# Kernel optimization log

Hardware: AMD Instinct MI355X
Metric: run time of the kernel (lower is better)

Reference implementation:

```python
import jax, jax.numpy as jnp
import numpy as np

N_NODES = 50000
N_EDGES = 600000
D_IN = 128
H = D_IN // 2  # 64
N_GRAPHS = 500
DIM_TARGET = 1


def setup_inputs() -> dict:
    key = jax.random.key(0)
    ks = jax.random.split(key, 16)
    x = jax.random.normal(ks[0], (N_NODES, D_IN), dtype=jnp.float32)
    edge_index = jax.random.randint(ks[1], (2, N_EDGES), 0, N_NODES, dtype=jnp.int64)
    batch = jnp.sort(jax.random.randint(ks[2], (N_NODES,), 0, N_GRAPHS, dtype=jnp.int64))
    # SAGEConv params: lin_l (neighbor aggregate, with bias), lin_r (root, no bias)
    s = 1.0 / np.sqrt(D_IN)
    Wl = jax.random.uniform(ks[3], (D_IN, H), jnp.float32, -s, s)
    bl = jnp.zeros((H,), jnp.float32)
    Wr = jax.random.uniform(ks[4], (D_IN, H), jnp.float32, -s, s)
    # MLP: 64->32->16->8->1
    dims = [H, H // 2, H // 4, H // 8, DIM_TARGET]
    params = {}
    for i in range(4):
        si = 1.0 / np.sqrt(dims[i])
        params[f"W{i}"] = jax.random.uniform(ks[5 + 2 * i], (dims[i], dims[i + 1]), jnp.float32, -si, si)
        params[f"b{i}"] = jax.random.uniform(ks[6 + 2 * i], (dims[i + 1],), jnp.float32, -si, si)
    return dict(x=x, edge_index=edge_index, batch=batch, Wl=Wl, bl=bl, Wr=Wr, **params)


def reference(x, edge_index, batch, Wl, bl, Wr, W0, b0, W1, b1, W2, b2, W3, b3):
    n_nodes = x.shape[0]
    src, dst = edge_index[0], edge_index[1]
    # SAGEConv mean aggregation: mean of source-node features at each target node
    agg = jax.ops.segment_sum(x[src], dst, num_segments=n_nodes)          # [N, D]
    cnt = jax.ops.segment_sum(jnp.ones((src.shape[0],), x.dtype), dst, num_segments=n_nodes)
    mean_nbr = agg / jnp.maximum(cnt, 1.0)[:, None]
    x1 = mean_nbr @ Wl + bl + x @ Wr                                      # [N, H]
    # global_mean_pool by graph id
    gsum = jax.ops.segment_sum(x1, batch, num_segments=N_GRAPHS)          # [G, H]
    gcnt = jax.ops.segment_sum(jnp.ones((n_nodes,), x.dtype), batch, num_segments=N_GRAPHS)
    h = gsum / jnp.maximum(gcnt, 1.0)[:, None]
    # MLP (dropout is identity in eval mode)
    h = jax.nn.relu(h @ W0 + b0)
    h = jax.nn.relu(h @ W1 + b1)
    h = jax.nn.relu(h @ W2 + b2)
    return h @ W3 + b3
```

## Files before the change

### kernel.cpp

```cpp
#include <hip/hip_runtime.h>
#include <hip/hip_bf16.h>

#define N_NODES  50000
#define N_EDGES  600000
#define D_IN     128
#define H        64
#define N_GRAPHS 500
#define MAXDEG   48

#define CONV_BLOCKS 6250
#define SCAT_CHUNKS 512
#define SCAT_BLOCKS (SCAT_CHUNKS * 8)
#define EPC         1172
#define NPS         (N_NODES / 8)
#define GST_BLOCKS  2
#define SPLIT       8

__device__ __forceinline__ float bflo(unsigned int u) { return __uint_as_float(u << 16); }
__device__ __forceinline__ float bfhi(unsigned int u) { return __uint_as_float(u & 0xffff0000u); }

__global__ __launch_bounds__(256) void prep_kernel(
        const float* __restrict__ x, unsigned short* __restrict__ xb,
        const int* __restrict__ src, const int* __restrict__ dst,
        int* __restrict__ deg, unsigned short* __restrict__ col,
        const int* __restrict__ batch, int* __restrict__ gstart) {
    int bid = blockIdx.x, t = threadIdx.x;
    if (bid < CONV_BLOCKS) {
        int i = bid * 256 + t;
        float4 f = ((const float4*)x)[i];
        ushort4 u;
        u.x = __bfloat16_as_ushort(__float2bfloat16(f.x));
        u.y = __bfloat16_as_ushort(__float2bfloat16(f.y));
        u.z = __bfloat16_as_ushort(__float2bfloat16(f.z));
        u.w = __bfloat16_as_ushort(__float2bfloat16(f.w));
        ((ushort4*)xb)[i] = u;
    } else if (bid < CONV_BLOCKS + SCAT_BLOCKS) {
        int rel   = bid - CONV_BLOCKS;
        int shard = bid & 7;
        int chunk = rel >> 3;
        int lo = shard * NPS, hi = lo + NPS;
        int e0 = chunk * EPC;
        int e1 = e0 + EPC; if (e1 > N_EDGES) e1 = N_EDGES;
        for (int e = e0 + t; e < e1; e += 256) {
            int d = dst[e];
            if (d >= lo && d < hi) {
                int pos = atomicAdd(&deg[d], 1);
                if (pos < MAXDEG)
                    col[(size_t)d * MAXDEG + pos] = (unsigned short)src[e];
            }
        }
    } else {
        int g = (bid - CONV_BLOCKS - SCAT_BLOCKS) * 256 + t;
        if (g <= N_GRAPHS) {
            int lo = 0, hi = N_NODES;
            while (lo < hi) {
                int m = (lo + hi) >> 1;
                if (batch[m] < g) lo = m + 1; else hi = m;
            }
            gstart[g] = lo;
        }
    }
}

__global__ __launch_bounds__(256) void gather_kernel(
        const unsigned short* __restrict__ xb, const unsigned short* __restrict__ col,
        const int* __restrict__ deg, const int* __restrict__ gstart,
        float* __restrict__ Pn, float* __restrict__ Px, int* __restrict__ gcnt) {
    __shared__ float red[4 * D_IN];
    int bid  = blockIdx.x;
    int wave = threadIdx.x >> 6;
    int lane = threadIdx.x & 63;

    if (bid < N_GRAPHS * SPLIT) {
        int g = bid >> 3;
        int s = bid & 7;
        int n0 = gstart[g], n1 = gstart[g + 1];
        const unsigned short* xl = xb + 2 * lane;

        float2 pn = make_float2(0.f, 0.f);
        for (int n = n0 + s * 4 + wave; n < n1; n += 4 * SPLIT) {
            int d = deg[n];
            int dl = (d < MAXDEG) ? d : MAXDEG;
            const unsigned short* cl = col + (size_t)n * MAXDEG;
            int cidx = (lane < dl) ? (int)cl[lane] : 0;

            float2 t = make_float2(0.f, 0.f);
            int j = 0;
            for (; j + 8 <= dl; j += 8) {
                int s0 = __shfl(cidx, j),     s1 = __shfl(cidx, j + 1);
                int s2 = __shfl(cidx, j + 2), s3 = __shfl(cidx, j + 3);
                int s4 = __shfl(cidx, j + 4), s5 = __shfl(cidx, j + 5);
                int s6 = __shfl(cidx, j + 6), s7 = __shfl(cidx, j + 7);
                unsigned int u0 = *(const unsigned int*)(xl + (size_t)s0 * D_IN);
                unsigned int u1 = *(const unsigned int*)(xl + (size_t)s1 * D_IN);
                unsigned int u2 = *(const unsigned int*)(xl + (size_t)s2 * D_IN);
                unsigned int u3 = *(const unsigned int*)(xl + (size_t)s3 * D_IN);
                unsigned int u4 = *(const unsigned int*)(xl + (size_t)s4 * D_IN);
                unsigned int u5 = *(const unsigned int*)(xl + (size_t)s5 * D_IN);
                unsigned int u6 = *(const unsigned int*)(xl + (size_t)s6 * D_IN);
                unsigned int u7 = *(const unsigned int*)(xl + (size_t)s7 * D_IN);
                t.x += bflo(u0) + bflo(u1) + bflo(u2) + bflo(u3)
                     + bflo(u4) + bflo(u5) + bflo(u6) + bflo(u7);
                t.y += bfhi(u0) + bfhi(u1) + bfhi(u2) + bfhi(u3)
                     + bfhi(u4) + bfhi(u5) + bfhi(u6) + bfhi(u7);
            }
            for (; j + 4 <= dl; j += 4) {
                int s0 = __shfl(cidx, j),     s1 = __shfl(cidx, j + 1);
                int s2 = __shfl(cidx, j + 2), s3 = __shfl(cidx, j + 3);
                unsigned int u0 = *(const unsigned int*)(xl + (size_t)s0 * D_IN);
                unsigned int u1 = *(const unsigned int*)(xl + (size_t)s1 * D_IN);
                unsigned int u2 = *(const unsigned int*)(xl + (size_t)s2 * D_IN);
                unsigned int u3 = *(const unsigned int*)(xl + (size_t)s3 * D_IN);
                t.x += bflo(u0) + bflo(u1) + bflo(u2) + bflo(u3);
                t.y += bfhi(u0) + bfhi(u1) + bfhi(u2) + bfhi(u3);
            }
            for (; j < dl; ++j) {
                int sn = __shfl(cidx, j);
                unsigned int u = *(const unsigned int*)(xl + (size_t)sn * D_IN);
                t.x += bflo(u); t.y += bfhi(u);
            }
            if (d > 0) {
                float w = __builtin_amdgcn_rcpf((float)d);
                pn.x = fmaf(t.x, w, pn.x);
                pn.y = fmaf(t.y, w, pn.y);
            }
        }
        red[wave * D_IN + 2 * lane]     = pn.x;
        red[wave * D_IN + 2 * lane + 1] = pn.y;
        __syncthreads();
        if (threadIdx.x < D_IN) {
            float v = red[threadIdx.x] + red[D_IN + threadIdx.x]
                    + red[2 * D_IN + threadIdx.x] + red[3 * D_IN + threadIdx.x];
            atomicAdd(&Pn[g * D_IN + threadIdx.x], v);
        }
    } else {
        int p  = bid - N_GRAPHS * SPLIT;
        int n0 = gstart[p], n1 = gstart[p + 1];
        float fx = 0.f, fy = 0.f;
        for (int n = n0 + wave; n < n1; n += 4) {
            unsigned int u = *(const unsigned int*)(xb + (size_t)n * D_IN + 2 * lane);
            fx += bflo(u); fy += bfhi(u);
        }
        red[wave * D_IN + 2 * lane]     = fx;
        red[wave * D_IN + 2 * lane + 1] = fy;
        __syncthreads();
        if (threadIdx.x < D_IN) {
            float v = red[threadIdx.x] + red[D_IN + threadIdx.x]
                    + red[2 * D_IN + threadIdx.x] + red[3 * D_IN + threadIdx.x];
            Px[p * D_IN + threadIdx.x] = v;
        }
        if (threadIdx.x == 0) gcnt[p] = n1 - n0;
    }
}

__global__ void final_kernel(
        const float* __restrict__ Pn, const float* __restrict__ Px,
        const int* __restrict__ gcnt,
        const float* __restrict__ Wl, const float* __restrict__ bl,
        const float* __restrict__ Wr,
        const float* __restrict__ W0, const float* __restrict__ b0,
        const float* __restrict__ W1, const float* __restrict__ b1,
        const float* __restrict__ W2, const float* __restrict__ b2,
        const float* __restrict__ W3, const float* __restrict__ b3,
        float* __restrict__ out) {
    int g = blockIdx.x;
    int t = threadIdx.x;
    __shared__ float sp[D_IN], sx[D_IN], h[H], a0[32], a1[16], a2[8];
    sp[t]      = Pn[g * D_IN + t];
    sp[t + 64] = Pn[g * D_IN + 64 + t];
    sx[t]      = Px[g * D_IN + t];
    sx[t + 64] = Px[g * D_IN + 64 + t];
    __syncthreads();

    int ng = gcnt[g];
    float acc = 0.f;
    #pragma unroll 8
    for (int d = 0; d < D_IN; ++d)
        acc += sp[d] * Wl[d * H + t] + sx[d] * Wr[d * H + t];
    h[t] = (ng > 0) ? (acc / (float)ng + bl[t]) : 0.f;
    __syncthreads();

    if (t < 32) { float a = b0[t]; for (int d = 0; d < H;  ++d) a += h[d]  * W0[d * 32 + t]; a0[t] = fmaxf(a, 0.f); }
    __syncthreads();
    if (t < 16) { float a = b1[t]; for (int d = 0; d < 32; ++d) a += a0[d] * W1[d * 16 + t]; a1[t] = fmaxf(a, 0.f); }
    __syncthreads();
    if (t < 8)  { float a = b2[t]; for (int d = 0; d < 16; ++d) a += a1[d] * W2[d * 8 + t];  a2[t] = fmaxf(a, 0.f); }
    __syncthreads();
    if (t == 0) { float a = b3[0]; for (int d = 0; d < 8;  ++d) a += a2[d] * W3[d]; out[g] = a; }
}

extern "C" void kernel_launch(void* const* d_in, const int* in_sizes, int n_in,
                              void* d_out, int out_size, void* d_ws, size_t ws_size,
                              hipStream_t stream) {
    const float* x     = (const float*)d_in[0];
    const int*   ei    = (const int*)  d_in[1];
    const int*   batch = (const int*)  d_in[2];
    const float* Wl    = (const float*)d_in[3];
    const float* bl    = (const float*)d_in[4];
    const float* Wr    = (const float*)d_in[5];
    const float* W0    = (const float*)d_in[6];
    const float* b0    = (const float*)d_in[7];
    const float* W1    = (const float*)d_in[8];
    const float* b1    = (const float*)d_in[9];
    const float* W2    = (const float*)d_in[10];
    const float* b2    = (const float*)d_in[11];
    const float* W3    = (const float*)d_in[12];
    const float* b3    = (const float*)d_in[13];
    float* out = (float*)d_out;

    char* ws = (char*)d_ws;
    int*            deg    = (int*)(ws + 0);
    float*          Pn     = (float*)(ws + 200704);
    float*          Px     = (float*)(ws + 460800);
    int*            gcnt   = (int*)(ws + 716800);
    int*            gstart = (int*)(ws + 720896);
    unsigned short* col    = (unsigned short*)(ws + 724992);
    unsigned short* xb     = (unsigned short*)(ws + 5524992);

    hipMemsetAsync(ws, 0, 456704, stream);

    prep_kernel<<<CONV_BLOCKS + SCAT_BLOCKS + GST_BLOCKS, 256, 0, stream>>>(
        x, xb, ei, ei + N_EDGES, deg, col, batch, gstart);
    gather_kernel<<<N_GRAPHS * SPLIT + N_GRAPHS, 256, 0, stream>>>(
        xb, col, deg, gstart, Pn, Px, gcnt);
    final_kernel<<<N_GRAPHS, 64, 0, stream>>>(Pn, Px, gcnt, Wl, bl, Wr,
                                              W0, b0, W1, b1, W2, b2, W3, b3, out);
}
```

Before: 165.4 us.

## Fuse final MLP into gather kernel via last-block ticket and per-split partials

Removes the separate final_kernel launch. The last-arriving block for each graph, found through an atomic ticket counter, runs the projection and the MLP. Per-split partial sums are now written to a private buffer instead of atomically added, and the last block reduces them. SPLIT doubles from 8 to 16 for more parallelism per graph. The memset shrinks to cover only deg and the done counters, at the cost of extra fences and a larger partial buffer.

```diff
diff --git a/kernel.cpp b/kernel.cpp
--- a/kernel.cpp
+++ b/kernel.cpp
@@ -14,7 +14,20 @@
 #define EPC         1172
 #define NPS         (N_NODES / 8)
 #define GST_BLOCKS  2
-#define SPLIT       8
+
+#define SPLIT    16
+#define GBLK     (N_GRAPHS * SPLIT)
+#define ARRIVALS (SPLIT + 1)
+
+#define OF_DEG   0
+#define OF_DONE  200704
+#define MEMSET_B 204800
+#define OF_PNP   204800
+#define OF_PX    4300800
+#define OF_GCNT  4556800
+#define OF_GST   4560000
+#define OF_COL   4562432
+#define OF_XB    9362432
 
 __device__ __forceinline__ float bflo(unsigned int u) { return __uint_as_float(u << 16); }
 __device__ __forceinline__ float bfhi(unsigned int u) { return __uint_as_float(u & 0xffff0000u); }
@@ -65,15 +78,27 @@
 __global__ __launch_bounds__(256) void gather_kernel(
         const unsigned short* __restrict__ xb, const unsigned short* __restrict__ col,
         const int* __restrict__ deg, const int* __restrict__ gstart,
-        float* __restrict__ Pn, float* __restrict__ Px, int* __restrict__ gcnt) {
+        float* __restrict__ PnP, float* __restrict__ Px, int* __restrict__ gcnt,
+        int* __restrict__ done,
+        const float* __restrict__ Wl, const float* __restrict__ bl,
+        const float* __restrict__ Wr,
+        const float* __restrict__ W0, const float* __restrict__ b0,
+        const float* __restrict__ W1, const float* __restrict__ b1,
+        const float* __restrict__ W2, const float* __restrict__ b2,
+        const float* __restrict__ W3, const float* __restrict__ b3,
+        float* __restrict__ out) {
     __shared__ float red[4 * D_IN];
+    __shared__ float sp[D_IN], sx[D_IN], hs[H], a0[32], a1[16], a2[8];
+    __shared__ int ticket;
     int bid  = blockIdx.x;
     int wave = threadIdx.x >> 6;
     int lane = threadIdx.x & 63;
-
-    if (bid < N_GRAPHS * SPLIT) {
-        int g = bid >> 3;
-        int s = bid & 7;
+    int G;
+
+    if (bid < GBLK) {
+        int g = bid >> 4;
+        int s = bid & 15;
+        G = g;
         int n0 = gstart[g], n1 = gstart[g + 1];
         const unsigned short* xl = xb + 2 * lane;
 
@@ -131,10 +156,11 @@
         if (threadIdx.x < D_IN) {
             float v = red[threadIdx.x] + red[D_IN + threadIdx.x]
                     + red[2 * D_IN + threadIdx.x] + red[3 * D_IN + threadIdx.x];
-            atomicAdd(&Pn[g * D_IN + threadIdx.x], v);
+            PnP[((size_t)bid) * D_IN + threadIdx.x] = v;
         }
     } else {
-        int p  = bid - N_GRAPHS * SPLIT;
+        int p  = bid - GBLK;
+        G = p;
         int n0 = gstart[p], n1 = gstart[p + 1];
         float fx = 0.f, fy = 0.f;
         for (int n = n0 + wave; n < n1; n += 4) {
@@ -147,46 +173,50 @@
         if (threadIdx.x < D_IN) {
             float v = red[threadIdx.x] + red[D_IN + threadIdx.x]
                     + red[2 * D_IN + threadIdx.x] + red[3 * D_IN + threadIdx.x];
-            Px[p * D_IN + threadIdx.x] = v;
+            Px[(size_t)p * D_IN + threadIdx.x] = v;
         }
         if (threadIdx.x == 0) gcnt[p] = n1 - n0;
     }
-}
-
-__global__ void final_kernel(
-        const float* __restrict__ Pn, const float* __restrict__ Px,
-        const int* __restrict__ gcnt,
-        const float* __restrict__ Wl, const float* __restrict__ bl,
-        const float* __restrict__ Wr,
-        const float* __restrict__ W0, const float* __restrict__ b0,
-        const float* __restrict__ W1, const float* __restrict__ b1,
-        const float* __restrict__ W2, const float* __restrict__ b2,
-        const float* __restrict__ W3, const float* __restrict__ b3,
-        float* __restrict__ out) {
-    int g = blockIdx.x;
-    int t = threadIdx.x;
-    __shared__ float sp[D_IN], sx[D_IN], h[H], a0[32], a1[16], a2[8];
-    sp[t]      = Pn[g * D_IN + t];
-    sp[t + 64] = Pn[g * D_IN + 64 + t];
-    sx[t]      = Px[g * D_IN + t];
-    sx[t + 64] = Px[g * D_IN + 64 + t];
+
     __syncthreads();
-
-    int ng = gcnt[g];
-    float acc = 0.f;
-    #pragma unroll 8
-    for (int d = 0; d < D_IN; ++d)
-        acc += sp[d] * Wl[d * H + t] + sx[d] * Wr[d * H + t];
-    h[t] = (ng > 0) ? (acc / (float)ng + bl[t]) : 0.f;
+    if (threadIdx.x == 0) {
+        __threadfence();
+        ticket = __hip_atomic_fetch_add(&done[G], 1, __ATOMIC_ACQ_REL,
+                                        __HIP_MEMORY_SCOPE_AGENT);
+    }
     __syncthreads();
-
-    if (t < 32) { float a = b0[t]; for (int d = 0; d < H;  ++d) a += h[d]  * W0[d * 32 + t]; a0[t] = fmaxf(a, 0.f); }
-    __syncthreads();
-    if (t < 16) { float a = b1[t]; for (int d = 0; d < 32; ++d) a += a0[d] * W1[d * 16 + t]; a1[t] = fmaxf(a, 0.f); }
-    __syncthreads();
-    if (t < 8)  { float a = b2[t]; for (int d = 0; d < 16; ++d) a += a1[d] * W2[d * 8 + t];  a2[t] = fmaxf(a, 0.f); }
-    __syncthreads();
-    if (t == 0) { float a = b3[0]; for (int d = 0; d < 8;  ++d) a += a2[d] * W3[d]; out[g] = a; }
+    if (ticket != ARRIVALS - 1) return;
+    __threadfence();
+
+    {
+        int t = threadIdx.x;
+        if (t < D_IN) {
+            const float* base = PnP + ((size_t)G << 4) * D_IN + t;
+            float v = 0.f;
+            #pragma unroll
+            for (int s = 0; s < SPLIT; ++s) v += base[s * D_IN];
+            sp[t] = v;
+        } else {
+            sx[t - D_IN] = Px[(size_t)G * D_IN + (t - D_IN)];
+        }
+        __syncthreads();
+        int ng = gcnt[G];
+        if (t < H) {
+            float acc = 0.f;
+            #pragma unroll 8
+            for (int d = 0; d < D_IN; ++d)
+                acc += sp[d] * Wl[d * H + t] + sx[d] * Wr[d * H + t];
+            hs[t] = (ng > 0) ? (acc / (float)ng + bl[t]) : 0.f;
+        }
+        __syncthreads();
+        if (t < 32) { float a = b0[t]; for (int d = 0; d < H;  ++d) a += hs[d] * W0[d * 32 + t]; a0[t] = fmaxf(a, 0.f); }
+        __syncthreads();
+        if (t < 16) { float a = b1[t]; for (int d = 0; d < 32; ++d) a += a0[d] * W1[d * 16 + t]; a1[t] = fmaxf(a, 0.f); }
+        __syncthreads();
+        if (t < 8)  { float a = b2[t]; for (int d = 0; d < 16; ++d) a += a1[d] * W2[d * 8 + t];  a2[t] = fmaxf(a, 0.f); }
+        __syncthreads();
+        if (t == 0) { float a = b3[0]; for (int d = 0; d < 8;  ++d) a += a2[d] * W3[d]; out[G] = a; }
+    }
 }
 
 extern "C" void kernel_launch(void* const* d_in, const int* in_sizes, int n_in,
@@ -209,20 +239,20 @@
     float* out = (float*)d_out;
 
     char* ws = (char*)d_ws;
-    int*            deg    = (int*)(ws + 0);
-    float*          Pn     = (float*)(ws + 200704);
-    float*          Px     = (float*)(ws + 460800);
-    int*            gcnt   = (int*)(ws + 716800);
-    int*            gstart = (int*)(ws + 720896);
-    unsigned short* col    = (unsigned short*)(ws + 724992);
-    unsigned short* xb     = (unsigned short*)(ws + 5524992);
-
-    hipMemsetAsync(ws, 0, 456704, stream);
+    int*            deg    = (int*)(ws + OF_DEG);
+    int*            done   = (int*)(ws + OF_DONE);
+    float*          PnP    = (float*)(ws + OF_PNP);
+    float*          Px     = (float*)(ws + OF_PX);
+    int*            gcnt   = (int*)(ws + OF_GCNT);
+    int*            gstart = (int*)(ws + OF_GST);
+    unsigned short* col    = (unsigned short*)(ws + OF_COL);
+    unsigned short* xb     = (unsigned short*)(ws + OF_XB);
+
+    hipMemsetAsync(ws, 0, MEMSET_B, stream);
 
     prep_kernel<<<CONV_BLOCKS + SCAT_BLOCKS + GST_BLOCKS, 256, 0, stream>>>(
         x, xb, ei, ei + N_EDGES, deg, col, batch, gstart);
-    gather_kernel<<<N_GRAPHS * SPLIT + N_GRAPHS, 256, 0, stream>>>(
-        xb, col, deg, gstart, Pn, Px, gcnt);
-    final_kernel<<<N_GRAPHS, 64, 0, stream>>>(Pn, Px, gcnt, Wl, bl, Wr,
-                                              W0, b0, W1, b1, W2, b2, W3, b3, out);
+    gather_kernel<<<GBLK + N_GRAPHS, 256, 0, stream>>>(
+        xb, col, deg, gstart, PnP, Px, gcnt, done,
+        Wl, bl, Wr, W0, b0, W1, b1, W2, b2, W3, b3, out);
 }
```

After: 595.0 us. 3.6x slower.
